# Performance work log

Hardware: AMD Instinct MI355X
Metric: run time of the kernel (lower is better)

The kernel has to match this reference:

```python
import jax, jax.numpy as jnp
import numpy as np

N_SPK = 2048
M_UTT = 16
D_EMB = 512
EPS = 1e-8  # torch cosine_similarity eps


def setup_inputs() -> dict:
    key = jax.random.key(0)
    k1, = jax.random.split(key, 1)
    speaker_vectors = jax.random.normal(k1, (N_SPK * M_UTT, D_EMB), dtype=jnp.float32)
    return {
        "speaker_vectors": speaker_vectors,
        "w": jnp.float32(10.0),
        "b": jnp.float32(-5.0),
        "speakers": N_SPK,
    }


def _normalize(x):
    # torch.cosine_similarity clamps each norm at eps
    n = jnp.maximum(jnp.linalg.norm(x, axis=-1, keepdims=True), EPS)
    return x / n


def reference(speaker_vectors, w, b, speakers):
    N = speakers
    NM, D = speaker_vectors.shape
    M = NM // N
    v3 = speaker_vectors.reshape(N, M, D)
    ssum = v3.sum(axis=1)                         # [N, D] per-speaker sums
    C = ssum / M                                  # full centroids [N, D]
    C_min = (ssum[:, None, :] - v3) / (M - 1)     # leave-one-out centroids [N, M, D]

    vn = _normalize(speaker_vectors)              # [NM, D]
    # diagonal similarities: cos(C_min[j], v[j]) per utterance j
    S_diag = jnp.sum(_normalize(C_min.reshape(NM, D)) * vn, axis=-1)  # [NM]
    # full similarity matrix via one normalized matmul: [N, NM]
    S_full = _normalize(C) @ vn.T
    # replace each speaker's own block row entries with leave-one-out sims
    col_spk = jnp.arange(NM) // M                 # speaker id of each column
    same = col_spk[None, :] == jnp.arange(N)[:, None]  # [N, NM]
    S = jnp.where(same, S_diag[None, :], S_full)

    # L_j = -(w*S_diag_j + b) + log sum_n exp(w*S[n,j] + b)
    L = -(w * S_diag + b) + jax.nn.logsumexp(w * S + b, axis=0)
    return L.sum()
```

## Files before the change

kernel.cpp:

```cpp
#include <hip/hip_runtime.h>
#include <stdint.h>

#define N_SPK 2048
#define M_UTT 16
#define D_EMB 512
#define NM (N_SPK * M_UTT)
#define FP8_SCALE 16.0f

typedef __attribute__((ext_vector_type(4))) float f32x4;
typedef __attribute__((ext_vector_type(4))) int   i32x4;
typedef __attribute__((ext_vector_type(8))) int   i32x8;

__device__ __forceinline__ void async_copy16(const void* g, void* l) {
    __builtin_amdgcn_global_load_lds(
        (const __attribute__((address_space(1))) unsigned int*)g,
        (__attribute__((address_space(3))) unsigned int*)l,
        16, 0, 0);
}

__device__ __forceinline__ i32x8 ld_frag(const unsigned char* base, int s0) {
    i32x4 lo = *(const i32x4*)(base + s0 * 16);
    i32x4 hi = *(const i32x4*)(base + (s0 ^ 1) * 16);
    return __builtin_shufflevector(lo, hi, 0, 1, 2, 3, 4, 5, 6, 7);
}

__global__ __launch_bounds__(256) void prep_kernel(
    const float* __restrict__ V, const float* __restrict__ wp,
    const float* __restrict__ bp, unsigned char* __restrict__ Cn8,
    unsigned char* __restrict__ vn8, float* __restrict__ dterm,
    float* __restrict__ colsum, float* __restrict__ out)
{
    const int spk = blockIdx.x, t = threadIdx.x;
    const int wave = t >> 6, lane = t & 63;
    const float2* vb = (const float2*)(V + (size_t)spk * (M_UTT * D_EMB));

    __shared__ __align__(16) float red[32][264];
    __shared__ float red2[32];
    __shared__ float invs[M_UTT];
    __shared__ float wred[4];

    if (spk < 128) colsum[spk * 256 + t] = 0.f;
    if (spk == 0 && t == 0) out[0] = 0.f;

    float2 p[M_UTT];
#pragma unroll
    for (int m = 0; m < M_UTT; ++m) p[m] = vb[m * 256 + t];

    float2 ss = make_float2(0.f, 0.f);
#pragma unroll
    for (int m = 0; m < M_UTT; ++m) { ss.x += p[m].x; ss.y += p[m].y; }

    float cnp = ss.x * ss.x + ss.y * ss.y;
#pragma unroll
    for (int off = 32; off > 0; off >>= 1) cnp += __shfl_xor(cnp, off);
    if (lane == 0) wred[wave] = cnp;

#pragma unroll
    for (int m = 0; m < M_UTT; ++m) {
        red[m][t]         = ss.x * p[m].x + ss.y * p[m].y;
        red[m + M_UTT][t] = p[m].x * p[m].x + p[m].y * p[m].y;
    }
    __syncthreads();
    const float cn2 = wred[0] + wred[1] + wred[2] + wred[3];

    {
        const int r = t >> 3, s = t & 7;
        const float4* rp = (const float4*)red;
        float4 a = make_float4(0.f, 0.f, 0.f, 0.f);
#pragma unroll
        for (int k = 0; k < 8; ++k) {
            float4 q = rp[r * 66 + s + 8 * k];
            a.x += q.x; a.y += q.y; a.z += q.z; a.w += q.w;
        }
        float v1 = (a.x + a.y) + (a.z + a.w);
        v1 += __shfl_xor(v1, 1);
        v1 += __shfl_xor(v1, 2);
        v1 += __shfl_xor(v1, 4);
        if (s == 0) red2[r] = v1;
    }
    __syncthreads();

    if (t < M_UTT) {
        const float sv = red2[t], vv = red2[t + M_UTT];
        const float cc = cn2 - 2.f * sv + vv;
        const float cv = sv - vv;
        const float dc = fmaxf(sqrtf(fmaxf(cc, 0.f)) * (1.f / (M_UTT - 1)), 1e-8f) * (M_UTT - 1);
        const float dv = fmaxf(sqrtf(vv), 1e-8f);
        dterm[spk * M_UTT + t] = (*wp) * (cv / (dc * dv)) + (*bp);
        invs[t] = FP8_SCALE / dv;
    }
    __syncthreads();

    const float cs = FP8_SCALE / (M_UTT * fmaxf(sqrtf(cn2) * (1.f / M_UTT), 1e-8f));
    {
        int pk = __builtin_amdgcn_cvt_pk_fp8_f32(ss.x * cs, ss.y * cs, 0, false);
        ((unsigned short*)(Cn8 + (size_t)spk * D_EMB))[t] = (unsigned short)pk;
    }
#pragma unroll
    for (int m = 0; m < M_UTT; ++m) {
        const float iv = invs[m];
        int pk = __builtin_amdgcn_cvt_pk_fp8_f32(p[m].x * iv, p[m].y * iv, 0, false);
        ((unsigned short*)(vn8 + ((size_t)(spk * M_UTT + m)) * D_EMB))[t] = (unsigned short)pk;
    }
}

__global__ __launch_bounds__(256) void gemm_kernel(
    const unsigned char* __restrict__ Cn8, const unsigned char* __restrict__ vn8,
    const float* __restrict__ wp, const float* __restrict__ bp,
    float* __restrict__ colsum)
{
    __shared__ __align__(16) unsigned char As[128 * 256];
    __shared__ __align__(16) unsigned char Bs[128 * 256];
    __shared__ float csum[128];

    const int tid = threadIdx.x;
    const int w = tid >> 6, l = tid & 63;
    const int d = blockIdx.x;
    const int xcd = d & 7, s = d >> 3;
    const int bx = xcd * 32 + (s >> 4);
    const int by = s & 15;
    const float wgt2 = (*wp) * (1.44269504f / (FP8_SCALE * FP8_SCALE));
    const float bsc2 = (*bp) * 1.44269504f;

    if (tid < 128) csum[tid] = 0.f;

    const int r_l = l >> 4, hh = (l >> 3) & 1, sl8 = l & 7;
    const int g_even = sl8 ^ r_l;
    const size_t rowoff = (size_t)(w * 32 + r_l) * D_EMB + hh * 128;
    const unsigned char* Ab0 = Cn8 + (size_t)(by * 128) * D_EMB + rowoff + g_even * 16;
    const unsigned char* Ab1 = Cn8 + (size_t)(by * 128) * D_EMB + rowoff + (g_even ^ 4) * 16;
    const unsigned char* Bb0 = vn8 + (size_t)(bx * 128) * D_EMB + rowoff + g_even * 16;
    const unsigned char* Bb1 = vn8 + (size_t)(bx * 128) * D_EMB + rowoff + (g_even ^ 4) * 16;
    unsigned char* AsW = As + (w * 32) * 256;
    unsigned char* BsW = Bs + (w * 32) * 256;

    const int wm = w & 1, wn = w >> 1;
    const int l16 = l & 15, q = l >> 4;
    const int s0 = (2 * q) ^ (l & 7);
    const unsigned char* Ard = As + (wm * 64 + l16) * 256;
    const unsigned char* Brd = Bs + (wn * 64 + l16) * 256;

    f32x4 acc[4][4];
    const f32x4 z = {0.f, 0.f, 0.f, 0.f};
#pragma unroll
    for (int i = 0; i < 4; ++i)
#pragma unroll
        for (int j = 0; j < 4; ++j) acc[i][j] = z;

#pragma unroll
    for (int kk = 0; kk < D_EMB; kk += 256) {
        __syncthreads();
#pragma unroll
        for (int i = 0; i < 8; ++i) {
            const unsigned char* pa = ((i & 1) ? Ab1 : Ab0) + i * 2048 + kk;
            const unsigned char* pb = ((i & 1) ? Bb1 : Bb0) + i * 2048 + kk;
            async_copy16(pa, AsW + i * 1024);
            async_copy16(pb, BsW + i * 1024);
        }
        __syncthreads();
#pragma unroll
        for (int h2 = 0; h2 < 2; ++h2) {
            const int ho = h2 * 128;
            i32x8 bfr[4];
#pragma unroll
            for (int j = 0; j < 4; ++j) bfr[j] = ld_frag(Brd + j * 4096 + ho, s0);
#pragma unroll
            for (int i = 0; i < 4; ++i) {
                i32x8 af = ld_frag(Ard + i * 4096 + ho, s0);
#pragma unroll
                for (int j = 0; j < 4; ++j)
                    acc[i][j] = __builtin_amdgcn_mfma_scale_f32_16x16x128_f8f6f4(
                        af, bfr[j], acc[i][j], 0, 0, 0, 0x7F7F7F7F, 0, 0x7F7F7F7F);
            }
        }
    }

    const int rowg0 = by * 128 + wm * 64 + q * 4;
    const int colg0 = bx * 128 + wn * 64 + l16;
#pragma unroll
    for (int j = 0; j < 4; ++j) {
        const int colg = colg0 + j * 16;
        const int cspk = colg >> 4;
        float p = 0.f;
#pragma unroll
        for (int i = 0; i < 4; ++i) {
            const int rowg = rowg0 + i * 16;
#pragma unroll
            for (int r = 0; r < 4; ++r) {
                float e = exp2f(fmaf(wgt2, acc[i][j][r], bsc2));
                p += (rowg + r == cspk) ? 0.f : e;
            }
        }
        p += __shfl_xor(p, 16);
        p += __shfl_xor(p, 32);
        if (q == 0) atomicAdd(&csum[wn * 64 + j * 16 + l16], p);
    }
    __syncthreads();
    if (tid < 128) atomicAdd(&colsum[bx * 128 + tid], csum[tid]);
}

__global__ __launch_bounds__(256) void finish_kernel(
    const float* __restrict__ dterm, const float* __restrict__ colsum,
    float* __restrict__ out)
{
    const int idx = blockIdx.x * 256 + threadIdx.x;
    const int stride = gridDim.x * 256;
    float local = 0.f;
    for (int j = idx; j < NM; j += stride) {
        float t = dterm[j];
        local += logf(colsum[j] + __expf(t)) - t;
    }
#pragma unroll
    for (int off = 32; off > 0; off >>= 1) local += __shfl_xor(local, off);
    __shared__ float wr[4];
    const int wave = threadIdx.x >> 6, lane = threadIdx.x & 63;
    if (lane == 0) wr[wave] = local;
    __syncthreads();
    if (threadIdx.x == 0) atomicAdd(out, wr[0] + wr[1] + wr[2] + wr[3]);
}

extern "C" void kernel_launch(void* const* d_in, const int* in_sizes, int n_in,
                              void* d_out, int out_size, void* d_ws, size_t ws_size,
                              hipStream_t stream) {
    const float* V  = (const float*)d_in[0];
    const float* wp = (const float*)d_in[1];
    const float* bp = (const float*)d_in[2];

    char* ws = (char*)d_ws;
    unsigned char* Cn8 = (unsigned char*)ws;
    unsigned char* vn8 = (unsigned char*)(ws + ((size_t)1 << 20));
    float* dterm  = (float*)(ws + ((size_t)17 << 20));
    float* colsum = dterm + NM;
    float* out    = (float*)d_out;

    prep_kernel<<<N_SPK, 256, 0, stream>>>(V, wp, bp, Cn8, vn8, dterm, colsum, out);
    gemm_kernel<<<4096, 256, 0, stream>>>(Cn8, vn8, wp, bp, colsum);
    finish_kernel<<<64, 256, 0, stream>>>(dterm, colsum, out);
}
```

Before: 153.0 us.

## Load GEMM MFMA fragments directly from global memory instead of LDS staging

Removes the LDS staging of the FP8 A and B tiles (async global-to-LDS copies plus two barriers per K step) in the GEMM kernel. Each lane now reads its 32-byte MFMA fragments straight from global memory (L2/L1 cached) every 128-wide K step. This frees 64KB of LDS per block, which may raise occupancy, and drops the synchronisation. In exchange the tiles are no longer shared through LDS, so each wave reloads its own data from cache, which adds global traffic and exposes load latency with no explicit prefetch.

```diff
diff --git a/kernel.cpp b/kernel.cpp
--- a/kernel.cpp
+++ b/kernel.cpp
@@ -8,21 +8,7 @@
 #define FP8_SCALE 16.0f
 
 typedef __attribute__((ext_vector_type(4))) float f32x4;
-typedef __attribute__((ext_vector_type(4))) int   i32x4;
 typedef __attribute__((ext_vector_type(8))) int   i32x8;
-
-__device__ __forceinline__ void async_copy16(const void* g, void* l) {
-    __builtin_amdgcn_global_load_lds(
-        (const __attribute__((address_space(1))) unsigned int*)g,
-        (__attribute__((address_space(3))) unsigned int*)l,
-        16, 0, 0);
-}
-
-__device__ __forceinline__ i32x8 ld_frag(const unsigned char* base, int s0) {
-    i32x4 lo = *(const i32x4*)(base + s0 * 16);
-    i32x4 hi = *(const i32x4*)(base + (s0 ^ 1) * 16);
-    return __builtin_shufflevector(lo, hi, 0, 1, 2, 3, 4, 5, 6, 7);
-}
 
 __global__ __launch_bounds__(256) void prep_kernel(
     const float* __restrict__ V, const float* __restrict__ wp,
@@ -109,8 +95,6 @@
     const float* __restrict__ wp, const float* __restrict__ bp,
     float* __restrict__ colsum)
 {
-    __shared__ __align__(16) unsigned char As[128 * 256];
-    __shared__ __align__(16) unsigned char Bs[128 * 256];
     __shared__ float csum[128];
 
     const int tid = threadIdx.x;
@@ -123,22 +107,12 @@
     const float bsc2 = (*bp) * 1.44269504f;
 
     if (tid < 128) csum[tid] = 0.f;
-
-    const int r_l = l >> 4, hh = (l >> 3) & 1, sl8 = l & 7;
-    const int g_even = sl8 ^ r_l;
-    const size_t rowoff = (size_t)(w * 32 + r_l) * D_EMB + hh * 128;
-    const unsigned char* Ab0 = Cn8 + (size_t)(by * 128) * D_EMB + rowoff + g_even * 16;
-    const unsigned char* Ab1 = Cn8 + (size_t)(by * 128) * D_EMB + rowoff + (g_even ^ 4) * 16;
-    const unsigned char* Bb0 = vn8 + (size_t)(bx * 128) * D_EMB + rowoff + g_even * 16;
-    const unsigned char* Bb1 = vn8 + (size_t)(bx * 128) * D_EMB + rowoff + (g_even ^ 4) * 16;
-    unsigned char* AsW = As + (w * 32) * 256;
-    unsigned char* BsW = Bs + (w * 32) * 256;
+    __syncthreads();
 
     const int wm = w & 1, wn = w >> 1;
     const int l16 = l & 15, q = l >> 4;
-    const int s0 = (2 * q) ^ (l & 7);
-    const unsigned char* Ard = As + (wm * 64 + l16) * 256;
-    const unsigned char* Brd = Bs + (wn * 64 + l16) * 256;
+    const unsigned char* Arow = Cn8 + (size_t)(by * 128 + wm * 64 + l16) * D_EMB + q * 32;
+    const unsigned char* Brow = vn8 + (size_t)(bx * 128 + wn * 64 + l16) * D_EMB + q * 32;
 
     f32x4 acc[4][4];
     const f32x4 z = {0.f, 0.f, 0.f, 0.f};
@@ -148,31 +122,20 @@
         for (int j = 0; j < 4; ++j) acc[i][j] = z;
 
 #pragma unroll
-    for (int kk = 0; kk < D_EMB; kk += 256) {
-        __syncthreads();
-#pragma unroll
-        for (int i = 0; i < 8; ++i) {
-            const unsigned char* pa = ((i & 1) ? Ab1 : Ab0) + i * 2048 + kk;
-            const unsigned char* pb = ((i & 1) ? Bb1 : Bb0) + i * 2048 + kk;
-            async_copy16(pa, AsW + i * 1024);
-            async_copy16(pb, BsW + i * 1024);
-        }
-        __syncthreads();
-#pragma unroll
-        for (int h2 = 0; h2 < 2; ++h2) {
-            const int ho = h2 * 128;
-            i32x8 bfr[4];
-#pragma unroll
-            for (int j = 0; j < 4; ++j) bfr[j] = ld_frag(Brd + j * 4096 + ho, s0);
-#pragma unroll
-            for (int i = 0; i < 4; ++i) {
-                i32x8 af = ld_frag(Ard + i * 4096 + ho, s0);
-#pragma unroll
-                for (int j = 0; j < 4; ++j)
-                    acc[i][j] = __builtin_amdgcn_mfma_scale_f32_16x16x128_f8f6f4(
-                        af, bfr[j], acc[i][j], 0, 0, 0, 0x7F7F7F7F, 0, 0x7F7F7F7F);
-            }
-        }
+    for (int kk = 0; kk < D_EMB; kk += 128) {
+        i32x8 af[4], bf[4];
+#pragma unroll
+        for (int i = 0; i < 4; ++i)
+            af[i] = *(const i32x8*)(Arow + (size_t)(i * 16) * D_EMB + kk);
+#pragma unroll
+        for (int j = 0; j < 4; ++j)
+            bf[j] = *(const i32x8*)(Brow + (size_t)(j * 16) * D_EMB + kk);
+#pragma unroll
+        for (int i = 0; i < 4; ++i)
+#pragma unroll
+            for (int j = 0; j < 4; ++j)
+                acc[i][j] = __builtin_amdgcn_mfma_scale_f32_16x16x128_f8f6f4(
+                    af[i], bf[j], acc[i][j], 0, 0, 0, 0x7F7F7F7F, 0, 0x7F7F7F7F);
     }
 
     const int rowg0 = by * 128 + wm * 64 + q * 4;
```

New measurement: 215.5 us. +40.8%, slower.
